# Kernel optimization log

Measured on AMD Instinct MI355X. Metric: run time of the kernel, lower is better.

The kernel has to match this reference:

```python
import jax, jax.numpy as jnp
import numpy as np

N = 8192       # node_num
F_IN = 256     # src_feature
F_OUT = 128    # out_feature
NEG_SLOPE = 0.2  # standard GAT leakyrelu slope
MASK_VAL = -1e12


def setup_inputs() -> dict:
    key = jax.random.key(0)
    k1, k2, k3, k4, k5, k6 = jax.random.split(key, 6)
    x = jax.random.normal(k1, (N, F_IN), dtype=jnp.float32)
    adj = jax.random.randint(k2, (N, N), 0, 2, dtype=jnp.int32)  # 0/1 adjacency mask
    # xavier-uniform-like scales
    W = jax.random.normal(k3, (F_IN, F_OUT), dtype=jnp.float32) * np.float32(1.0 / np.sqrt(F_IN))
    a1 = jax.random.normal(k4, (F_OUT,), dtype=jnp.float32) * np.float32(0.1)  # att[:F_OUT]
    a2 = jax.random.normal(k5, (F_OUT,), dtype=jnp.float32) * np.float32(0.1)  # att[F_OUT:]
    bias = jax.random.normal(k6, (F_OUT,), dtype=jnp.float32) * np.float32(0.1)
    return {"x": x, "adj": adj, "W": W, "a1": a1, "a2": a2, "bias": bias}


def reference(x, adj, W, a1, a2, bias):
    # h = x @ W1  (src_h == dst_h for int src_dst_feature)
    h = x @ W  # [N, F_OUT]
    # e[i,j] = leakyrelu(att^T [h_i || h_j]) decomposed as (h@a1)_i + (h@a2)_j
    s_src = h @ a1  # [N]
    s_dst = h @ a2  # [N]
    e = jax.nn.leaky_relu(s_src[:, None] + s_dst[None, :], NEG_SLOPE)  # [N, N]
    masked = jnp.where(adj > 0, e, jnp.float32(MASK_VAL))
    attention = jax.nn.softmax(masked, axis=1)  # [N, N]
    # dropout in eval mode = identity; aggregate neighbor features
    out = attention @ h + bias  # [N, F_OUT]
    return out
```

## Files before the change

kernel.cpp:

```cpp
#include <hip/hip_runtime.h>
#include <cstdint>
#include <cstddef>

#define NN 8192
#define FIN 256
#define FOUT 128
#define SLOPE 0.2f
#define SHIFT 8.0f

typedef float f32x4 __attribute__((ext_vector_type(4)));
typedef __bf16 bf16x8 __attribute__((ext_vector_type(8)));
typedef int i32x4 __attribute__((ext_vector_type(4)));
typedef unsigned int u32x4 __attribute__((ext_vector_type(4)));

__device__ __forceinline__ unsigned short f2bf(float f) {
  return __builtin_bit_cast(unsigned short, (__bf16)f);
}

__device__ __forceinline__ void async_cp16(void* lds, const void* g) {
  __builtin_amdgcn_global_load_lds(
      (const __attribute__((address_space(1))) void*)g,
      (__attribute__((address_space(3))) void*)lds, 16, 0, 0);
}

__global__ __launch_bounds__(256, 4) void k_hw(const float* __restrict__ x,
                                               const float* __restrict__ W,
                                               const float* __restrict__ a1,
                                               const float* __restrict__ a2,
                                               unsigned short* __restrict__ ht,
                                               float* __restrict__ Etab,
                                               unsigned short* __restrict__ FbfF,
                                               unsigned short* __restrict__ FbfF2) {
  __shared__ float xs[8][256];
  __shared__ unsigned short tile[128][8];
  const int tid = threadIdx.x;
  const int rowbase = blockIdx.x * 8;

  #pragma unroll
  for (int it = 0; it < 2; ++it) {
    int fi = it * 1024 + tid * 4;
    int r = fi >> 8, k = fi & 255;
    *(f32x4*)&xs[r][k] = *(const f32x4*)(x + (size_t)(rowbase + r) * FIN + k);
  }
  __syncthreads();

  const int r = tid >> 5;
  const int cg = tid & 31;
  f32x4 acc = {0.f, 0.f, 0.f, 0.f};

  #pragma unroll 8
  for (int k = 0; k < FIN; ++k) {
    f32x4 wv = *(const f32x4*)(W + k * FOUT + cg * 4);
    float xv = xs[r][k];
    acc[0] += xv * wv[0];
    acc[1] += xv * wv[1];
    acc[2] += xv * wv[2];
    acc[3] += xv * wv[3];
  }

  #pragma unroll
  for (int c = 0; c < 4; ++c) tile[cg * 4 + c][r] = f2bf(acc[c]);

  f32x4 av1 = *(const f32x4*)(a1 + cg * 4);
  f32x4 av2 = *(const f32x4*)(a2 + cg * 4);
  float s1 = acc[0] * av1[0] + acc[1] * av1[1] + acc[2] * av1[2] + acc[3] * av1[3];
  float s2 = acc[0] * av2[0] + acc[1] * av2[1] + acc[2] * av2[2] + acc[3] * av2[3];
  #pragma unroll
  for (int off = 16; off > 0; off >>= 1) {
    s1 += __shfl_xor(s1, off, 64);
    s2 += __shfl_xor(s2, off, 64);
  }
  if (cg == 0) {
    const int row = rowbase + r;
    float c0 = s1 + SHIFT;
    float c = fmaxf(c0, SLOPE * c0);
    Etab[(size_t)row * 2]     = __expf(s1 - c);
    Etab[(size_t)row * 2 + 1] = __expf(SLOPE * s1 - c);
    FbfF[row]  = f2bf(__expf(s2));
    FbfF2[row] = f2bf(__expf(SLOPE * s2));
  }
  __syncthreads();

  if (tid < 128) {
    u32x4 v = *(const u32x4*)&tile[tid][0];
    *(u32x4*)(ht + (size_t)tid * NN + rowbase) = v;
  }
}

__global__ __launch_bounds__(256, 2) void k_gat(const int* __restrict__ adj,
                                                const unsigned short* __restrict__ ht,
                                                const float* __restrict__ Etab,
                                                const unsigned short* __restrict__ FbfF,
                                                const unsigned short* __restrict__ FbfF2,
                                                const float* __restrict__ bias,
                                                float* __restrict__ out) {
  __shared__ int sA[2][16 * 64];
  __shared__ unsigned short sH[2][128 * 64];
  __shared__ unsigned short sF[2][128];

  const int tid = threadIdx.x;
  const int wave = tid >> 6;
  const int lane = tid & 63;
  const int quad = lane >> 4;
  const int m = lane & 15;
  const int rowbase = blockIdx.x * 16;
  const int row = rowbase + m;

  bf16x8 pm, pinv, pones;
  #pragma unroll
  for (int jj = 0; jj < 8; ++jj) {
    pm[jj] = (__bf16)(float)m;
    pinv[jj] = (__bf16)0.03125f;
    pones[jj] = (__bf16)1.0f;
  }
  f32x4 z = {0.f, 0.f, 0.f, 0.f};
  f32x4 rp = __builtin_amdgcn_mfma_f32_16x16x32_bf16(pm, pinv, z, 0, 0, 0);
  f32x4 cp = __builtin_amdgcn_mfma_f32_16x16x32_bf16(pinv, pm, z, 0, 0, 0);
  int rowmap[4], colmap[4];
  #pragma unroll
  for (int r = 0; r < 4; ++r) {
    rowmap[r] = ((int)(rp[r] + 0.5f)) & 15;
    colmap[r] = ((int)(cp[r] + 0.5f)) & 15;
  }

  const float E  = Etab[(size_t)row * 2];
  const float E2 = Etab[(size_t)row * 2 + 1];

  const int t0 = wave * 2, t1 = wave * 2 + 1;

  f32x4 acc0 = z, acc1 = z, den = z;

  const unsigned short* srcH[4];
  #pragma unroll
  for (int il = 0; il < 4; ++il) {
    const int i = wave * 4 + il;
    const int f = i * 8 + (lane >> 3);
    const int g = (lane & 7) ^ (lane >> 3);
    srcH[il] = ht + (size_t)f * NN + g * 8;
  }
  const int* srcA[2] = {nullptr, nullptr};
  int slotA[2] = {0, 0};
  if (wave >= 2) {
    #pragma unroll
    for (int q = 0; q < 2; ++q) {
      const int il = (wave - 2) * 2 + q;
      const int r = il * 4 + (lane >> 4);
      const int g = (lane & 15) ^ r;
      slotA[q] = il;
      srcA[q] = adj + (size_t)(rowbase + r) * NN + g * 4;
    }
  }
  const unsigned short* srcF = nullptr;
  if (wave == 1) {
    srcF = (lane < 8) ? (FbfF + lane * 8) : (FbfF2 + (lane - 8) * 8);
  }

  auto stage = [&](int b) {
    #pragma unroll
    for (int il = 0; il < 4; ++il) {
      async_cp16(&sH[b][(wave * 4 + il) * 512], srcH[il]);
      srcH[il] += 64;
    }
    if (wave >= 2) {
      #pragma unroll
      for (int q = 0; q < 2; ++q) {
        async_cp16(&sA[b][slotA[q] * 256], srcA[q]);
        srcA[q] += 64;
      }
    } else if (wave == 1 && lane < 16) {
      async_cp16(&sF[b][0], srcF);
      srcF += 64;
    }
  };

  stage(0);

  for (int c = 0; c < 128; ++c) {
    const int cs = c & 1, ns = cs ^ 1;

    __syncthreads();
    if (c + 1 < 128) stage(ns);

    #pragma unroll
    for (int k32 = 0; k32 < 2; ++k32) {
      const int g0 = k32 * 8 + quad * 2;
      i32x4 A0 = *(const i32x4*)&sA[cs][m * 64 + ((g0) ^ m) * 4];
      i32x4 A1 = *(const i32x4*)&sA[cs][m * 64 + ((g0 + 1) ^ m) * 4];
      const int jl = k32 * 32 + quad * 8;
      u32x4 Fq = *(const u32x4*)&sF[cs][jl];
      u32x4 Gq = *(const u32x4*)&sF[cs][64 + jl];

      bf16x8 af;
      #pragma unroll
      for (int p = 0; p < 4; ++p) {
        const unsigned fp = Fq[p], gp = Gq[p];
        const float Flo = __builtin_bit_cast(float, fp << 16);
        const float Fhi = __builtin_bit_cast(float, fp & 0xffff0000u);
        const float Glo = __builtin_bit_cast(float, gp << 16);
        const float Ghi = __builtin_bit_cast(float, gp & 0xffff0000u);
        const float wlo = fmaxf(E * Flo, E2 * Glo);
        const float whi = fmaxf(E * Fhi, E2 * Ghi);
        const int avlo = (p < 2) ? A0[p * 2] : A1[p * 2 - 4];
        const int avhi = (p < 2) ? A0[p * 2 + 1] : A1[p * 2 - 3];
        af[p * 2]     = avlo ? (__bf16)wlo : (__bf16)0.0f;
        af[p * 2 + 1] = avhi ? (__bf16)whi : (__bf16)0.0f;
      }

      const int s0 = (k32 * 4 + quad) ^ (m & 7);
      bf16x8 b0 = __builtin_bit_cast(bf16x8,
          *(const u32x4*)&sH[cs][(t0 * 16 + m) * 64 + s0 * 8]);
      bf16x8 b1 = __builtin_bit_cast(bf16x8,
          *(const u32x4*)&sH[cs][(t1 * 16 + m) * 64 + s0 * 8]);

      acc0 = __builtin_amdgcn_mfma_f32_16x16x32_bf16(af, b0, acc0, 0, 0, 0);
      acc1 = __builtin_amdgcn_mfma_f32_16x16x32_bf16(af, b1, acc1, 0, 0, 0);
      den  = __builtin_amdgcn_mfma_f32_16x16x32_bf16(af, pones, den, 0, 0, 0);
    }
  }

  #pragma unroll
  for (int r = 0; r < 4; ++r) {
    const float inv = 1.0f / den[r];
    const int orow = rowbase + rowmap[r];
    const int c0 = t0 * 16 + colmap[r];
    const int c1 = t1 * 16 + colmap[r];
    out[(size_t)orow * FOUT + c0] = acc0[r] * inv + bias[c0];
    out[(size_t)orow * FOUT + c1] = acc1[r] * inv + bias[c1];
  }
}

extern "C" void kernel_launch(void* const* d_in, const int* in_sizes, int n_in,
                              void* d_out, int out_size, void* d_ws, size_t ws_size,
                              hipStream_t stream) {
  const float* x    = (const float*)d_in[0];
  const int*   adj  = (const int*)d_in[1];
  const float* W    = (const float*)d_in[2];
  const float* a1   = (const float*)d_in[3];
  const float* a2   = (const float*)d_in[4];
  const float* bias = (const float*)d_in[5];
  float* out = (float*)d_out;

  char* ws = (char*)d_ws;
  unsigned short* ht = (unsigned short*)ws;
  float* Etab = (float*)(ws + (size_t)2 * 1024 * 1024);
  unsigned short* FbfF =
      (unsigned short*)(ws + (size_t)2 * 1024 * 1024 + 64 * 1024);
  unsigned short* FbfF2 = FbfF + NN;

  k_hw<<<NN / 8, 256, 0, stream>>>(x, W, a1, a2, ht, Etab, FbfF, FbfF2);
  k_gat<<<NN / 16, 256, 0, stream>>>(adj, ht, Etab, FbfF, FbfF2, bias, out);
}
```

Baseline: 478.2 us.

## Split GAT columns across two blocks, load adjacency directly to registers

The attention aggregation kernel now splits the 8192 neighbor columns into two halves handled by separate blocks, doubling the grid. Partial numerators and softmax denominators are combined with float atomics into a zeroed output and workspace, and a final kernel normalizes and adds bias. Adjacency is no longer staged through LDS but loaded straight into registers with a manual double-buffered loop, and occupancy hint is raised to 4. This adds two extra launches and atomic traffic in exchange for more parallelism and less LDS pressure.

```diff
diff --git a/kernel.cpp b/kernel.cpp
--- a/kernel.cpp
+++ b/kernel.cpp
@@ -87,14 +87,21 @@
   }
 }
 
-__global__ __launch_bounds__(256, 2) void k_gat(const int* __restrict__ adj,
+__global__ __launch_bounds__(256) void k_zero(float* __restrict__ outacc,
+                                              float* __restrict__ dws) {
+  const int i = blockIdx.x * 256 + threadIdx.x;
+  f32x4 z = {0.f, 0.f, 0.f, 0.f};
+  ((f32x4*)outacc)[i] = z;
+  if (i < NN / 4) ((f32x4*)dws)[i] = z;
+}
+
+__global__ __launch_bounds__(256, 4) void k_gat(const int* __restrict__ adj,
                                                 const unsigned short* __restrict__ ht,
                                                 const float* __restrict__ Etab,
                                                 const unsigned short* __restrict__ FbfF,
                                                 const unsigned short* __restrict__ FbfF2,
-                                                const float* __restrict__ bias,
-                                                float* __restrict__ out) {
-  __shared__ int sA[2][16 * 64];
+                                                float* __restrict__ outacc,
+                                                float* __restrict__ dws) {
   __shared__ unsigned short sH[2][128 * 64];
   __shared__ unsigned short sF[2][128];
 
@@ -103,7 +110,8 @@
   const int lane = tid & 63;
   const int quad = lane >> 4;
   const int m = lane & 15;
-  const int rowbase = blockIdx.x * 16;
+  const int rowbase = (int)(blockIdx.x >> 1) * 16;
+  const int colbase = (int)(blockIdx.x & 1) * (NN / 2);
   const int row = rowbase + m;
 
   bf16x8 pm, pinv, pones;
@@ -125,7 +133,6 @@
 
   const float E  = Etab[(size_t)row * 2];
   const float E2 = Etab[(size_t)row * 2 + 1];
-
   const int t0 = wave * 2, t1 = wave * 2 + 1;
 
   f32x4 acc0 = z, acc1 = z, den = z;
@@ -136,23 +143,12 @@
     const int i = wave * 4 + il;
     const int f = i * 8 + (lane >> 3);
     const int g = (lane & 7) ^ (lane >> 3);
-    srcH[il] = ht + (size_t)f * NN + g * 8;
-  }
-  const int* srcA[2] = {nullptr, nullptr};
-  int slotA[2] = {0, 0};
-  if (wave >= 2) {
-    #pragma unroll
-    for (int q = 0; q < 2; ++q) {
-      const int il = (wave - 2) * 2 + q;
-      const int r = il * 4 + (lane >> 4);
-      const int g = (lane & 15) ^ r;
-      slotA[q] = il;
-      srcA[q] = adj + (size_t)(rowbase + r) * NN + g * 4;
-    }
+    srcH[il] = ht + (size_t)f * NN + colbase + g * 8;
   }
   const unsigned short* srcF = nullptr;
   if (wave == 1) {
-    srcF = (lane < 8) ? (FbfF + lane * 8) : (FbfF2 + (lane - 8) * 8);
+    srcF = (lane < 8) ? (FbfF + colbase + lane * 8)
+                      : (FbfF2 + colbase + (lane - 8) * 8);
   }
 
   auto stage = [&](int b) {
@@ -161,34 +157,29 @@
       async_cp16(&sH[b][(wave * 4 + il) * 512], srcH[il]);
       srcH[il] += 64;
     }
-    if (wave >= 2) {
-      #pragma unroll
-      for (int q = 0; q < 2; ++q) {
-        async_cp16(&sA[b][slotA[q] * 256], srcA[q]);
-        srcA[q] += 64;
-      }
-    } else if (wave == 1 && lane < 16) {
+    if (wave == 1 && lane < 16) {
       async_cp16(&sF[b][0], srcF);
       srcF += 64;
     }
   };
 
-  stage(0);
-
-  for (int c = 0; c < 128; ++c) {
-    const int cs = c & 1, ns = cs ^ 1;
-
-    __syncthreads();
-    if (c + 1 < 128) stage(ns);
-
+  const int* arow = adj + (size_t)row * NN + colbase + quad * 8;
+  auto load_adj = [&](i32x4* d, int c) {
+    const int* p = arow + c * 64;
+    d[0] = *(const i32x4*)(p);
+    d[1] = *(const i32x4*)(p + 4);
+    d[2] = *(const i32x4*)(p + 32);
+    d[3] = *(const i32x4*)(p + 36);
+  };
+
+  auto compute = [&](int cs, const i32x4* av) {
     #pragma unroll
     for (int k32 = 0; k32 < 2; ++k32) {
-      const int g0 = k32 * 8 + quad * 2;
-      i32x4 A0 = *(const i32x4*)&sA[cs][m * 64 + ((g0) ^ m) * 4];
-      i32x4 A1 = *(const i32x4*)&sA[cs][m * 64 + ((g0 + 1) ^ m) * 4];
       const int jl = k32 * 32 + quad * 8;
       u32x4 Fq = *(const u32x4*)&sF[cs][jl];
       u32x4 Gq = *(const u32x4*)&sF[cs][64 + jl];
+      const i32x4 A0 = av[k32 * 2];
+      const i32x4 A1 = av[k32 * 2 + 1];
 
       bf16x8 af;
       #pragma unroll
@@ -216,17 +207,56 @@
       acc1 = __builtin_amdgcn_mfma_f32_16x16x32_bf16(af, b1, acc1, 0, 0, 0);
       den  = __builtin_amdgcn_mfma_f32_16x16x32_bf16(af, pones, den, 0, 0, 0);
     }
+  };
+
+  i32x4 aA[4], aB[4];
+  load_adj(aA, 0);
+  stage(0);
+
+  #pragma unroll 1
+  for (int c = 0; c < 64; c += 2) {
+    __syncthreads();
+    stage(1);
+    load_adj(aB, c + 1);
+    compute(0, aA);
+    __syncthreads();
+    if (c + 2 < 64) {
+      stage(0);
+      load_adj(aA, c + 2);
+    }
+    compute(1, aB);
   }
 
   #pragma unroll
   for (int r = 0; r < 4; ++r) {
-    const float inv = 1.0f / den[r];
     const int orow = rowbase + rowmap[r];
     const int c0 = t0 * 16 + colmap[r];
     const int c1 = t1 * 16 + colmap[r];
-    out[(size_t)orow * FOUT + c0] = acc0[r] * inv + bias[c0];
-    out[(size_t)orow * FOUT + c1] = acc1[r] * inv + bias[c1];
-  }
+    atomicAdd(&outacc[(size_t)orow * FOUT + c0], acc0[r]);
+    atomicAdd(&outacc[(size_t)orow * FOUT + c1], acc1[r]);
+  }
+  if (wave == 0 && m == 0) {
+    #pragma unroll
+    for (int r = 0; r < 4; ++r) {
+      atomicAdd(&dws[rowbase + rowmap[r]], den[r]);
+    }
+  }
+}
+
+__global__ __launch_bounds__(256) void k_fin(const float* __restrict__ dws,
+                                             const float* __restrict__ bias,
+                                             float* __restrict__ out) {
+  const int idx = (blockIdx.x * 256 + threadIdx.x) * 4;
+  const int rowi = idx >> 7;
+  const int f = idx & 127;
+  const float inv = 1.0f / dws[rowi];
+  f32x4 v = *(f32x4*)(out + idx);
+  f32x4 b = *(const f32x4*)(bias + f);
+  v[0] = v[0] * inv + b[0];
+  v[1] = v[1] * inv + b[1];
+  v[2] = v[2] * inv + b[2];
+  v[3] = v[3] * inv + b[3];
+  *(f32x4*)(out + idx) = v;
 }
 
 extern "C" void kernel_launch(void* const* d_in, const int* in_sizes, int n_in,
@@ -246,7 +276,10 @@
   unsigned short* FbfF =
       (unsigned short*)(ws + (size_t)2 * 1024 * 1024 + 64 * 1024);
   unsigned short* FbfF2 = FbfF + NN;
-
+  float* dws = (float*)(ws + (size_t)2 * 1024 * 1024 + 96 * 1024);
+
+  k_zero<<<(NN * FOUT / 4) / 256, 256, 0, stream>>>(out, dws);
   k_hw<<<NN / 8, 256, 0, stream>>>(x, W, a1, a2, ht, Etab, FbfF, FbfF2);
-  k_gat<<<NN / 16, 256, 0, stream>>>(adj, ht, Etab, FbfF, FbfF2, bias, out);
-}
+  k_gat<<<(NN / 16) * 2, 256, 0, stream>>>(adj, ht, Etab, FbfF, FbfF2, out, dws);
+  k_fin<<<(NN * FOUT / 4) / 256, 256, 0, stream>>>(dws, bias, out);
+}
```

Measured after the change: 509.3 us. 1.06x slower.
